# Performance work log

Measured on AMD Instinct MI355X. Metric: run time of the kernel, lower is better.

Reference implementation:

```python
import jax, jax.numpy as jnp
import numpy as np


def setup_inputs() -> dict:
    key = jax.random.key(0)
    k1, k2 = jax.random.split(key)
    B, M, N, D = 8, 2048, 2048, 1024
    x = jax.random.normal(k1, (B, M, D), dtype=jnp.float32)
    y = jax.random.normal(k2, (B, N, D), dtype=jnp.float32)
    return {"x": x, "y": y}


def reference(x, y):
    # scores e[b,m,n] = <x[b,m], y[b,n]>   (K.batch_dot(x, y, axes=2))
    e = jnp.einsum('bmd,bnd->bmn', x, y)
    # stable softmax over last axis (the exp/max/sum sequence in the original)
    p = jax.nn.softmax(e, axis=-1)
    # K.batch_dot(z, x, axes=1): contract axis 1 (m) of both -> [B, n, d]; V = x
    out = jnp.einsum('bmn,bmd->bnd', p, x)
    return out
```

## Files before the change

kernel.cpp:

```cpp
#include <hip/hip_runtime.h>
#include <hip/hip_bf16.h>
#include <stdint.h>

#define B_ 8
#define M_ 2048
#define N_ 2048
#define D_ 1024

typedef __bf16 bf16x8 __attribute__((ext_vector_type(8)));
typedef float f32x4 __attribute__((ext_vector_type(4)));
typedef uint16_t us4 __attribute__((ext_vector_type(4)));
typedef uint16_t us8 __attribute__((ext_vector_type(8)));

__device__ __forceinline__ uint16_t f2b(float f) {
    uint32_t u = __float_as_uint(f);
    return (uint16_t)((u + 0x7FFFu + ((u >> 16) & 1u)) >> 16);
}
__device__ __forceinline__ float b2f(uint16_t h) {
    return __uint_as_float(((uint32_t)h) << 16);
}

__device__ __forceinline__ void gld16(const uint16_t* g, const uint16_t* l) {
    __builtin_amdgcn_global_load_lds(
        (const __attribute__((address_space(1))) uint32_t*)g,
        (__attribute__((address_space(3))) uint32_t*)l,
        16, 0, 0);
}

__global__ __launch_bounds__(256) void k_split(const float* __restrict__ x,
                                               const float* __restrict__ y,
                                               uint16_t* __restrict__ xh, uint16_t* __restrict__ xl,
                                               uint16_t* __restrict__ yh, uint16_t* __restrict__ yl) {
    const int i = (blockIdx.x * 256 + threadIdx.x) * 4;
    float4 vx = *(const float4*)(x + i);
    float4 vy = *(const float4*)(y + i);
    float fx[4] = {vx.x, vx.y, vx.z, vx.w};
    float fy[4] = {vy.x, vy.y, vy.z, vy.w};
    us4 hx, lx, hy, ly;
#pragma unroll
    for (int k = 0; k < 4; ++k) {
        uint16_t h = f2b(fx[k]);
        hx[k] = h; lx[k] = f2b(fx[k] - b2f(h));
        uint16_t g = f2b(fy[k]);
        hy[k] = g; ly[k] = f2b(fy[k] - b2f(g));
    }
    *(us4*)(xh + i) = hx;
    *(us4*)(xl + i) = lx;
    *(us4*)(yh + i) = hy;
    *(us4*)(yl + i) = ly;
}

#define SBAR0 __builtin_amdgcn_sched_barrier(0)
#define LD8(off) (*(const bf16x8*)&lds[off])
#define RDB(bo)                                                        \
    _Pragma("unroll") for (int j = 0; j < 4; ++j) {                    \
        bh[j] = LD8((bo) + bbase + j * 512);                           \
        bl[j] = LD8((bo) + bbase + 8192 + j * 512);                    \
    }
#define RDA(H, L, bo, q)                                               \
    H[0] = LD8((bo) + abase + ((q)*2) * 512);                          \
    H[1] = LD8((bo) + abase + ((q)*2 + 1) * 512);                      \
    L[0] = LD8((bo) + abase + 8192 + ((q)*2) * 512);                   \
    L[1] = LD8((bo) + abase + 8192 + ((q)*2 + 1) * 512);
#define MMQ(H, L, q)                                                   \
    __builtin_amdgcn_s_setprio(1);                                     \
    _Pragma("unroll") for (int ii = 0; ii < 2; ++ii)                   \
    _Pragma("unroll") for (int j = 0; j < 4; ++j) {                    \
        acc[(q)*2 + ii][j] = __builtin_amdgcn_mfma_f32_16x16x32_bf16(  \
            H[ii], bh[j], acc[(q)*2 + ii][j], 0, 0, 0);                \
        acc[(q)*2 + ii][j] = __builtin_amdgcn_mfma_f32_16x16x32_bf16(  \
            H[ii], bl[j], acc[(q)*2 + ii][j], 0, 0, 0);                \
        acc[(q)*2 + ii][j] = __builtin_amdgcn_mfma_f32_16x16x32_bf16(  \
            L[ii], bh[j], acc[(q)*2 + ii][j], 0, 0, 0);                \
    }                                                                  \
    __builtin_amdgcn_s_setprio(0);

__global__ __launch_bounds__(512, 2) void k_gemm1(const uint16_t* __restrict__ xh,
                                                  const uint16_t* __restrict__ xl,
                                                  const uint16_t* __restrict__ yh,
                                                  const uint16_t* __restrict__ yl,
                                                  float* __restrict__ e,
                                                  float* __restrict__ pmax,
                                                  float* __restrict__ psum) {
    const int b = blockIdx.z;
    const int m0 = blockIdx.x * 256;
    const int n0 = blockIdx.y * 256;
    __shared__ __align__(16) uint16_t lds[65536];

    const int tid = threadIdx.x;
    const int lane = tid & 63;
    const int wid = tid >> 6;
    const int wm = (wid >> 2) * 128;
    const int wn = (wid & 3) * 64;
    const int quad = lane >> 4;
    const int r16 = lane & 15;
    const int swz8 = (quad ^ ((r16 >> 1) & 3)) * 8;

    const int base_row = wid * 16 + (lane >> 2);
    const int gd8 = ((lane & 3) ^ ((lane >> 3) & 3)) * 8;
    const uint16_t* gp[4];
    gp[0] = xh + ((size_t)b * M_ + m0 + base_row) * D_ + gd8;
    gp[1] = xl + ((size_t)b * M_ + m0 + base_row) * D_ + gd8;
    gp[2] = yh + ((size_t)b * N_ + n0 + base_row) * D_ + gd8;
    gp[3] = yl + ((size_t)b * N_ + n0 + base_row) * D_ + gd8;
    const int ldsW = wid * 512;

    const int abase = (wm + r16) * 32 + swz8;
    const int bbase = 16384 + (wn + r16) * 32 + swz8;

    auto STAGE = [&](int dst, int ktn) {
#pragma unroll
        for (int c = 0; c < 8; ++c)
            gld16(gp[c >> 1] + (size_t)(c & 1) * (128 * D_) + ktn * 32,
                  &lds[dst + c * 4096 + ldsW]);
    };

    f32x4 acc[8][4];
#pragma unroll
    for (int i = 0; i < 8; ++i)
#pragma unroll
        for (int j = 0; j < 4; ++j) acc[i][j] = (f32x4){0.f, 0.f, 0.f, 0.f};

    bf16x8 bh[4], bl[4];
    bf16x8 a0h[2], a0l[2];
    bf16x8 a1h[2], a1l[2];

    STAGE(0, 0);
    asm volatile("s_waitcnt vmcnt(0)" ::: "memory");
    SBAR0; __builtin_amdgcn_s_barrier(); SBAR0;
    RDB(0); RDA(a0h, a0l, 0, 0);

    for (int t = 0; t < 32; ++t) {
        const int bo = (t & 1) << 15;
        const int nbo = bo ^ 32768;
        const bool more = t < 31;

        if (more) STAGE(nbo, t + 1);
        RDA(a1h, a1l, bo, 1);
        SBAR0;
        MMQ(a0h, a0l, 0);
        SBAR0;

        RDA(a0h, a0l, bo, 2);
        SBAR0;
        MMQ(a1h, a1l, 1);
        SBAR0;

        RDA(a1h, a1l, bo, 3);
        SBAR0;
        MMQ(a0h, a0l, 2);
        SBAR0;

        asm volatile("s_waitcnt vmcnt(0)" ::: "memory");
        SBAR0; __builtin_amdgcn_s_barrier(); SBAR0;

        if (more) { RDA(a0h, a0l, nbo, 0); }
        SBAR0;
        MMQ(a1h, a1l, 3);
        SBAR0;
        if (more) {
            RDB(nbo);
            SBAR0; __builtin_amdgcn_s_barrier(); SBAR0;
        }
    }

    float* eb = e + (size_t)b * M_ * N_;
    const int grows = (int)gridDim.z * M_;
    const int growbase = b * M_ + m0 + wm;
    const int nb = (n0 + wn) >> 6;
    float* pm = pmax + (size_t)nb * grows + growbase;
    float* ps = psum + (size_t)nb * grows + growbase;

#pragma unroll
    for (int i = 0; i < 8; ++i) {
#pragma unroll
        for (int r = 0; r < 4; ++r) {
            const float v0 = acc[i][0][r], v1 = acc[i][1][r];
            const float v2 = acc[i][2][r], v3 = acc[i][3][r];
            float mrow = fmaxf(fmaxf(v0, v1), fmaxf(v2, v3));
#pragma unroll
            for (int s = 1; s < 16; s <<= 1) mrow = fmaxf(mrow, __shfl_xor(mrow, s, 64));
            float srow_ = __expf(v0 - mrow) + __expf(v1 - mrow)
                        + __expf(v2 - mrow) + __expf(v3 - mrow);
#pragma unroll
            for (int s = 1; s < 16; s <<= 1) srow_ += __shfl_xor(srow_, s, 64);
            const int lrow = i * 16 + quad * 4 + r;
            if (r16 == 0) { pm[lrow] = mrow; ps[lrow] = srow_; }
            const size_t ebase = (size_t)(m0 + wm + lrow) * N_ + n0 + wn + r16;
#pragma unroll
            for (int j = 0; j < 4; ++j) eb[ebase + j * 16] = acc[i][j][r];
        }
    }
}

__global__ __launch_bounds__(256) void k_combine(const float* __restrict__ pmax,
                                                 const float* __restrict__ psum,
                                                 float* __restrict__ mx,
                                                 float* __restrict__ inv, int rows) {
    const int r = blockIdx.x * 256 + threadIdx.x;
    float m = -3.4e38f;
#pragma unroll
    for (int nb = 0; nb < 32; ++nb) m = fmaxf(m, pmax[(size_t)nb * rows + r]);
    float s = 0.f;
#pragma unroll
    for (int nb = 0; nb < 32; ++nb)
        s += psum[(size_t)nb * rows + r] * __expf(pmax[(size_t)nb * rows + r] - m);
    mx[r] = m;
    inv[r] = 1.0f / s;
}

__global__ __launch_bounds__(256) void k_texp(const float* __restrict__ e,
                                              const float* __restrict__ mx,
                                              const float* __restrict__ inv,
                                              uint16_t* __restrict__ pT) {
    const int b = blockIdx.z, m0 = blockIdx.x * 64, n0 = blockIdx.y * 64;
    __shared__ float tile[64 * 65];
    const int t = threadIdx.x;
    const float* eb = e + (size_t)b * M_ * N_;
#pragma unroll
    for (int q = 0; q < 4; ++q) {
        const int row = q * 16 + (t >> 4);
        const int c4 = (t & 15) * 4;
        float4 v = *(const float4*)&eb[(size_t)(m0 + row) * N_ + n0 + c4];
        const float mv = mx[b * M_ + m0 + row];
        const float iv = inv[b * M_ + m0 + row];
        tile[row * 65 + c4 + 0] = __expf(v.x - mv) * iv;
        tile[row * 65 + c4 + 1] = __expf(v.y - mv) * iv;
        tile[row * 65 + c4 + 2] = __expf(v.z - mv) * iv;
        tile[row * 65 + c4 + 3] = __expf(v.w - mv) * iv;
    }
    __syncthreads();
    uint16_t* pb = pT + (size_t)b * N_ * M_;
#pragma unroll
    for (int q = 0; q < 2; ++q) {
        const int n = q * 32 + (t >> 3);
        const int mc = (t & 7) * 8;
        us8 o;
#pragma unroll
        for (int k = 0; k < 8; ++k) o[k] = f2b(tile[(mc + k) * 65 + n]);
        *(us8*)&pb[(size_t)(n0 + n) * M_ + m0 + mc] = o;
    }
}

__global__ __launch_bounds__(256) void k_tx(const uint16_t* __restrict__ xh,
                                            uint16_t* __restrict__ xt) {
    const int b = blockIdx.z, m0 = blockIdx.x * 64, d0 = blockIdx.y * 64;
    __shared__ float tile[64 * 65];
    const int t = threadIdx.x;
    const uint16_t* xb = xh + (size_t)b * M_ * D_;
#pragma unroll
    for (int q = 0; q < 2; ++q) {
        const int row = q * 32 + (t >> 3);
        const int c8 = (t & 7) * 8;
        us8 v = *(const us8*)&xb[(size_t)(m0 + row) * D_ + d0 + c8];
#pragma unroll
        for (int k = 0; k < 8; ++k) tile[row * 65 + c8 + k] = b2f(v[k]);
    }
    __syncthreads();
    uint16_t* xtb = xt + (size_t)b * D_ * M_;
#pragma unroll
    for (int q = 0; q < 2; ++q) {
        const int d = q * 32 + (t >> 3);
        const int mc = (t & 7) * 8;
        us8 o;
#pragma unroll
        for (int k = 0; k < 8; ++k) o[k] = f2b(tile[(mc + k) * 65 + d]);
        *(us8*)&xtb[(size_t)(d0 + d) * M_ + m0 + mc] = o;
    }
}

__global__ __launch_bounds__(256) void k_gemm2(const uint16_t* __restrict__ pT,
                                               const uint16_t* __restrict__ xt,
                                               float* __restrict__ out) {
    const int b = blockIdx.z;
    const int n0 = blockIdx.x * 128;
    const int d0 = blockIdx.y * 128;
    __shared__ __align__(16) uint16_t lds[32768];

    const int tid = threadIdx.x;
    const int lane = tid & 63;
    const int wid = tid >> 6;
    const int wn = (wid & 1) * 64;
    const int wd = (wid >> 1) * 64;
    const int quad = lane >> 4;
    const int r16 = lane & 15;

    const uint16_t* srcA = pT + ((size_t)b * N_ + n0) * M_;
    const uint16_t* srcB = xt + ((size_t)b * D_ + d0) * M_;

    f32x4 acc[4][4];
#pragma unroll
    for (int i = 0; i < 4; ++i)
#pragma unroll
        for (int j = 0; j < 4; ++j) acc[i][j] = (f32x4){0.f, 0.f, 0.f, 0.f};

    auto STAGE = [&](int dst, int kt) {
#pragma unroll
        for (int c = 0; c < 8; ++c) {
            const int offbase = c * 2048 + wid * 512;
            const int tile = offbase >> 13;
            const int o = (offbase & 8191) + lane * 8;
            const int row = o >> 6;
            const int gp = (o & 63) >> 3;
            const int gd = gp ^ (row & 7);
            const uint16_t* sp = tile ? srcB : srcA;
            gld16(sp + (size_t)row * M_ + kt * 64 + gd * 8, &lds[dst + offbase]);
        }
    };

    STAGE(0, 0);
    __syncthreads();

    for (int kt = 0; kt < M_ / 64; ++kt) {
        const int bo = (kt & 1) << 14;
        const int nbo = bo ^ 16384;
        if (kt < M_ / 64 - 1) STAGE(nbo, kt + 1);

#pragma unroll
        for (int h = 0; h < 2; ++h) {
            const int p = (h * 4 + quad) ^ (r16 & 7);
            bf16x8 a[4], bbr[4];
#pragma unroll
            for (int i = 0; i < 4; ++i) {
                a[i]   = *(const bf16x8*)&lds[bo + (wn + i * 16 + r16) * 64 + p * 8];
                bbr[i] = *(const bf16x8*)&lds[bo + 8192 + (wd + i * 16 + r16) * 64 + p * 8];
            }
#pragma unroll
            for (int i = 0; i < 4; ++i)
#pragma unroll
                for (int j = 0; j < 4; ++j)
                    acc[i][j] = __builtin_amdgcn_mfma_f32_16x16x32_bf16(a[i], bbr[j], acc[i][j], 0, 0, 0);
        }
        __syncthreads();
    }

    float* ob = out + (size_t)b * N_ * D_;
#pragma unroll
    for (int i = 0; i < 4; ++i) {
        const int rbase = n0 + wn + i * 16 + quad * 4;
#pragma unroll
        for (int j = 0; j < 4; ++j) {
            const int col = d0 + wd + j * 16 + r16;
#pragma unroll
            for (int r = 0; r < 4; ++r)
                ob[(size_t)(rbase + r) * D_ + col] = acc[i][j][r];
        }
    }
}

extern "C" void kernel_launch(void* const* d_in, const int* in_sizes, int n_in,
                              void* d_out, int out_size, void* d_ws, size_t ws_size,
                              hipStream_t stream) {
    const float* x = (const float*)d_in[0];
    const float* y = (const float*)d_in[1];
    float* out = (float*)d_out;
    char* ws = (char*)d_ws;

    const size_t MiB = 1024 * 1024;
    int g = 8;
    while (g > 1 && (size_t)g * 32 * MiB > ws_size) g >>= 1;
    if ((size_t)g * 32 * MiB > ws_size) return;

    const size_t T = (size_t)g * M_ * D_ * 2;
    uint16_t* xh = (uint16_t*)(ws + 0 * T);
    uint16_t* xl = (uint16_t*)(ws + 1 * T);
    uint16_t* yh = (uint16_t*)(ws + 2 * T);
    uint16_t* yl = (uint16_t*)(ws + 3 * T);
    float*    e  = (float*)(ws + 4 * T);
    uint16_t* xt = xl;
    uint16_t* pT = yh;

    const size_t pelems = (size_t)32 * g * M_;
    float* dtail = (float*)d_out + (size_t)B_ * N_ * D_;
    float* pmax = dtail - 2 * pelems;
    float* psum = pmax + pelems;
    float* mx   = dtail - 2 * pelems - 2 * (size_t)g * M_;
    float* inv  = mx + (size_t)g * M_;

    for (int c0 = 0; c0 < B_; c0 += g) {
        const float* xc = x + (size_t)c0 * M_ * D_;
        const float* yc = y + (size_t)c0 * N_ * D_;
        float* oc = out + (size_t)c0 * N_ * D_;

        hipLaunchKernelGGL(k_split, dim3((g * M_ * D_) / (256 * 4)), dim3(256), 0, stream,
                           xc, yc, xh, xl, yh, yl);
        hipLaunchKernelGGL(k_gemm1, dim3(M_ / 256, N_ / 256, g), dim3(512), 0, stream,
                           xh, xl, yh, yl, e, pmax, psum);
        hipLaunchKernelGGL(k_combine, dim3((g * M_) / 256), dim3(256), 0, stream,
                           pmax, psum, mx, inv, g * M_);
        hipLaunchKernelGGL(k_texp, dim3(M_ / 64, N_ / 64, g), dim3(256), 0, stream,
                           e, mx, inv, pT);
        hipLaunchKernelGGL(k_tx, dim3(M_ / 64, D_ / 64, g), dim3(256), 0, stream, xh, xt);
        hipLaunchKernelGGL(k_gemm2, dim3(N_ / 128, D_ / 128, g), dim3(256), 0, stream,
                           pT, xt, oc);
    }
}
```

Before: 467.6 us.

## Enlarge second GEMM tile to 256x256 with 512 threads and MFMA priority

The P^T·X GEMM moves from a 128x128 tile with 4 waves to a 256x256 tile with 8 waves. Each wave now computes 128x64 with an 8x4 accumulator array, and the staging index math and LDS buffers (128 KB double-buffered) are reworked to match. This raises arithmetic intensity per LDS/global byte loaded, and s_setprio is wrapped around the MFMA blocks to favour issue. In exchange it uses more registers and LDS per block, which lowers occupancy, and the grid has fewer blocks.

```diff
diff --git a/kernel.cpp b/kernel.cpp
--- a/kernel.cpp
+++ b/kernel.cpp
@@ -269,74 +269,77 @@
     }
 }
 
-__global__ __launch_bounds__(256) void k_gemm2(const uint16_t* __restrict__ pT,
-                                               const uint16_t* __restrict__ xt,
-                                               float* __restrict__ out) {
+__global__ __launch_bounds__(512, 2) void k_gemm2(const uint16_t* __restrict__ pT,
+                                                  const uint16_t* __restrict__ xt,
+                                                  float* __restrict__ out) {
     const int b = blockIdx.z;
-    const int n0 = blockIdx.x * 128;
-    const int d0 = blockIdx.y * 128;
-    __shared__ __align__(16) uint16_t lds[32768];
+    const int n0 = blockIdx.x * 256;
+    const int d0 = blockIdx.y * 256;
+    __shared__ __align__(16) uint16_t lds[65536];
 
     const int tid = threadIdx.x;
     const int lane = tid & 63;
     const int wid = tid >> 6;
-    const int wn = (wid & 1) * 64;
-    const int wd = (wid >> 1) * 64;
+    const int wn = (wid >> 2) * 128;
+    const int wd = (wid & 3) * 64;
     const int quad = lane >> 4;
     const int r16 = lane & 15;
 
     const uint16_t* srcA = pT + ((size_t)b * N_ + n0) * M_;
     const uint16_t* srcB = xt + ((size_t)b * D_ + d0) * M_;
 
-    f32x4 acc[4][4];
-#pragma unroll
-    for (int i = 0; i < 4; ++i)
-#pragma unroll
-        for (int j = 0; j < 4; ++j) acc[i][j] = (f32x4){0.f, 0.f, 0.f, 0.f};
+    const int srow = tid >> 3;
+    const int gd8 = ((tid & 7) ^ (srow & 7)) * 8;
+    const int ldsW = wid * 512;
 
     auto STAGE = [&](int dst, int kt) {
 #pragma unroll
         for (int c = 0; c < 8; ++c) {
-            const int offbase = c * 2048 + wid * 512;
-            const int tile = offbase >> 13;
-            const int o = (offbase & 8191) + lane * 8;
-            const int row = o >> 6;
-            const int gp = (o & 63) >> 3;
-            const int gd = gp ^ (row & 7);
-            const uint16_t* sp = tile ? srcB : srcA;
-            gld16(sp + (size_t)row * M_ + kt * 64 + gd * 8, &lds[dst + offbase]);
+            const uint16_t* sp = (c < 4) ? srcA : srcB;
+            const int r = (c & 3) * 64 + srow;
+            gld16(sp + (size_t)r * M_ + kt * 64 + gd8,
+                  &lds[dst + ((c < 4) ? 0 : 16384) + (c & 3) * 4096 + ldsW]);
         }
     };
 
+    f32x4 acc[8][4];
+#pragma unroll
+    for (int i = 0; i < 8; ++i)
+#pragma unroll
+        for (int j = 0; j < 4; ++j) acc[i][j] = (f32x4){0.f, 0.f, 0.f, 0.f};
+
     STAGE(0, 0);
     __syncthreads();
 
     for (int kt = 0; kt < M_ / 64; ++kt) {
-        const int bo = (kt & 1) << 14;
-        const int nbo = bo ^ 16384;
+        const int bo = (kt & 1) << 15;
+        const int nbo = bo ^ 32768;
         if (kt < M_ / 64 - 1) STAGE(nbo, kt + 1);
 
 #pragma unroll
         for (int h = 0; h < 2; ++h) {
             const int p = (h * 4 + quad) ^ (r16 & 7);
-            bf16x8 a[4], bbr[4];
-#pragma unroll
-            for (int i = 0; i < 4; ++i) {
-                a[i]   = *(const bf16x8*)&lds[bo + (wn + i * 16 + r16) * 64 + p * 8];
-                bbr[i] = *(const bf16x8*)&lds[bo + 8192 + (wd + i * 16 + r16) * 64 + p * 8];
-            }
-#pragma unroll
-            for (int i = 0; i < 4; ++i)
+            bf16x8 a[8], bbr[4];
+#pragma unroll
+            for (int i = 0; i < 8; ++i)
+                a[i] = *(const bf16x8*)&lds[bo + (wn + i * 16 + r16) * 64 + p * 8];
+#pragma unroll
+            for (int j = 0; j < 4; ++j)
+                bbr[j] = *(const bf16x8*)&lds[bo + 16384 + (wd + j * 16 + r16) * 64 + p * 8];
+            __builtin_amdgcn_s_setprio(1);
+#pragma unroll
+            for (int i = 0; i < 8; ++i)
 #pragma unroll
                 for (int j = 0; j < 4; ++j)
                     acc[i][j] = __builtin_amdgcn_mfma_f32_16x16x32_bf16(a[i], bbr[j], acc[i][j], 0, 0, 0);
+            __builtin_amdgcn_s_setprio(0);
         }
         __syncthreads();
     }
 
     float* ob = out + (size_t)b * N_ * D_;
 #pragma unroll
-    for (int i = 0; i < 4; ++i) {
+    for (int i = 0; i < 8; ++i) {
         const int rbase = n0 + wn + i * 16 + quad * 4;
 #pragma unroll
         for (int j = 0; j < 4; ++j) {
@@ -391,7 +394,7 @@
         hipLaunchKernelGGL(k_texp, dim3(M_ / 64, N_ / 64, g), dim3(256), 0, stream,
                            e, mx, inv, pT);
         hipLaunchKernelGGL(k_tx, dim3(M_ / 64, D_ / 64, g), dim3(256), 0, stream, xh, xt);
-        hipLaunchKernelGGL(k_gemm2, dim3(N_ / 128, D_ / 128, g), dim3(256), 0, stream,
+        hipLaunchKernelGGL(k_gemm2, dim3(N_ / 256, D_ / 256, g), dim3(512), 0, stream,
                            pT, xt, oc);
     }
 }
```

Result: no change. 458.8 us (-1.9%).
